# Kernel tuning notes

Hardware: AMD Instinct MI355X
Metric: run time of the kernel (lower is better)

Reference implementation:

```python
import jax, jax.numpy as jnp
import numpy as np

N_NODES = 100000
N_EDGES = 600000
D = 128


def gcn_conv(x, W, b, src, dst, n_nodes):
    """PyG-style GCNConv: add self-loops, symmetric deg^{-1/2} normalization."""
    xw = x @ W  # [N, out]
    # degree of destination nodes, counting the added self-loop
    deg = jnp.zeros((n_nodes,), xw.dtype).at[dst].add(1.0) + 1.0
    dinv = jax.lax.rsqrt(deg)
    coef = dinv[src] * dinv[dst]  # [E]
    agg = jnp.zeros_like(xw).at[dst].add(xw[src] * coef[:, None])
    agg = agg + xw * (dinv * dinv)[:, None]  # self-loop term
    return agg + b


def setup_inputs() -> dict:
    key = jax.random.key(0)
    k = jax.random.split(key, 9)
    s = 1.0 / np.sqrt(D)
    return {
        "x": jax.random.normal(k[0], (N_NODES, D), jnp.float32),
        "edge_index_pos": jax.random.randint(k[1], (2, N_EDGES), 0, N_NODES, jnp.int64),
        "edge_index_neg": jax.random.randint(k[2], (2, N_EDGES), 0, N_NODES, jnp.int64),
        "W1": jax.random.uniform(k[3], (D, D), jnp.float32, -s, s),
        "b1": jnp.zeros((D,), jnp.float32),
        "W2": jax.random.uniform(k[4], (D, D), jnp.float32, -s, s),
        "b2": jnp.zeros((D,), jnp.float32),
        "weight": jax.random.uniform(k[5], (2 * D, D), jnp.float32, -s, s),
        "bias": jnp.zeros((D,), jnp.float32),
    }


def reference(x, edge_index_pos, edge_index_neg, W1, b1, W2, b2, weight, bias):
    n = x.shape[0]
    h1 = gcn_conv(x, W1, b1, edge_index_pos[0], edge_index_pos[1], n)  # [N, D]
    h2 = gcn_conv(x, W2, b2, edge_index_neg[0], edge_index_neg[1], n)  # [N, D]
    h = jnp.concatenate([h1, h2], axis=-1)  # [N, 2D]
    return h @ weight + bias  # [N, D]
```

## Files before the change

kernel.cpp:

```cpp
#include <hip/hip_runtime.h>

#define N_NODES 100000
#define NT (2 * N_NODES)
#define D 128
#define N_EDGES 600000
#define ET (2 * N_EDGES)
#define SCAN_B 256
#define NBLK2 ((NT + SCAN_B - 1) / SCAN_B)
#define FROWS 256
#define FBLK ((N_NODES + FROWS - 1) / FROWS)
#define XBLK 12500
#define EGRID ((ET + 255) / 256)

typedef __attribute__((ext_vector_type(8))) short bf16x8;
typedef __attribute__((ext_vector_type(4))) float f32x4;

__device__ __forceinline__ unsigned short f2bf(float f) {
    union { float f; unsigned u; } v; v.f = f;
    unsigned r = (v.u + 0x7fff + ((v.u >> 16) & 1)) >> 16;
    return (unsigned short)r;
}
__device__ __forceinline__ float bf2f(unsigned short h) {
    union { unsigned u; float f; } v; v.u = ((unsigned)h) << 16;
    return v.f;
}

__device__ __forceinline__ long long load_idx(const void* e, long long i, int is32) {
    if (is32) return (long long)((const int*)e)[i];
    return ((const long long*)e)[i];
}

__device__ __forceinline__ int self_detect(const unsigned long long* __restrict__ e) {
    unsigned long long v = e[threadIdx.x & 63];
    unsigned long long m = __ballot(v > 0xFFFFFFFFull);
    return (m != 0ull) ? 1 : 0;
}

__global__ void prep_x2bf_degree(const float* __restrict__ W1, const float* __restrict__ W2,
                                 const float* __restrict__ weight,
                                 const float* __restrict__ b1, const float* __restrict__ b2,
                                 const float* __restrict__ bias,
                                 const float* __restrict__ x, unsigned short* __restrict__ xb,
                                 const void* __restrict__ ep, const void* __restrict__ en,
                                 unsigned short* __restrict__ Mt, float* __restrict__ bt,
                                 int* __restrict__ degi) {
    const int b = blockIdx.x;
    if (b < 128) {
        int idx = b * 256 + threadIdx.x;
        int j = idx >> 8, k = idx & 255;
        float a = 0.f;
        if (k < D) {
            for (int d = 0; d < D; ++d) a += W1[k * D + d] * weight[d * D + j];
        } else {
            for (int d = 0; d < D; ++d) a += W2[(k - D) * D + d] * weight[(D + d) * D + j];
        }
        Mt[j * 256 + k] = f2bf(a);
    } else if (b == 128) {
        int t = threadIdx.x;
        if (t < D) {
            float a = bias[t];
            for (int k = 0; k < D; ++k)
                a += b1[k] * weight[k * D + t] + b2[k] * weight[(D + k) * D + t];
            bt[t] = a;
        }
    } else if (b < 129 + XBLK) {
        long long t = (long long)(b - 129) * 256 + threadIdx.x;
        float4 a = ((const float4*)x)[t];
        ((ushort4*)xb)[t] = make_ushort4(f2bf(a.x), f2bf(a.y), f2bf(a.z), f2bf(a.w));
    } else {
        int is32 = self_detect((const unsigned long long*)ep);
        int i = (b - 129 - XBLK) * 256 + threadIdx.x;
        if (i >= ET) return;
        int conv = (i >= N_EDGES);
        const void* e = conv ? en : ep;
        int j = conv ? i - N_EDGES : i;
        long long d = load_idx(e, (long long)N_EDGES + j, is32);
        atomicAdd(&degi[conv * N_NODES + (int)d], 1);
    }
}

__global__ void scan_pass1(const int* __restrict__ degi, int* __restrict__ bsum,
                           float* __restrict__ dinv, unsigned char* __restrict__ degb) {
    __shared__ int sm[SCAN_B];
    int i = blockIdx.x * SCAN_B + threadIdx.x;
    int v = (i < NT) ? degi[i] : 0;
    if (i < NT) {
        dinv[i] = rsqrtf((float)v + 1.0f);
        degb[i] = (unsigned char)(v > 255 ? 255 : v);
    }
    sm[threadIdx.x] = v;
    __syncthreads();
    for (int s = SCAN_B / 2; s > 0; s >>= 1) {
        if (threadIdx.x < s) sm[threadIdx.x] += sm[threadIdx.x + s];
        __syncthreads();
    }
    if (threadIdx.x == 0) bsum[blockIdx.x] = sm[0];
}

__global__ void scan_pass3(const int* __restrict__ degi, const int* __restrict__ bsum,
                           int* __restrict__ off) {
    __shared__ int red[SCAN_B];
    __shared__ int sm[SCAN_B];
    int partial = 0;
    for (int i = threadIdx.x; i < blockIdx.x; i += SCAN_B) partial += bsum[i];
    red[threadIdx.x] = partial;
    __syncthreads();
    for (int s = SCAN_B / 2; s > 0; s >>= 1) {
        if (threadIdx.x < s) red[threadIdx.x] += red[threadIdx.x + s];
        __syncthreads();
    }
    int base = red[0];
    int i = blockIdx.x * SCAN_B + threadIdx.x;
    int v = (i < NT) ? degi[i] : 0;
    sm[threadIdx.x] = v;
    __syncthreads();
    for (int ofs = 1; ofs < SCAN_B; ofs <<= 1) {
        int add = (threadIdx.x >= ofs) ? sm[threadIdx.x - ofs] : 0;
        __syncthreads();
        sm[threadIdx.x] += add;
        __syncthreads();
    }
    int excl = sm[threadIdx.x] - v + base;
    if (i < NT) off[i] = excl;
    if (i == NT - 1) off[NT] = excl + v;
}

__global__ void csr_fill_both(const void* __restrict__ ep, const void* __restrict__ en,
                              const int* __restrict__ off,
                              int* __restrict__ degi, const unsigned char* __restrict__ degb,
                              unsigned* __restrict__ csr) {
    int is32 = self_detect((const unsigned long long*)ep);
    int i = blockIdx.x * blockDim.x + threadIdx.x;
    if (i >= ET) return;
    int conv = (i >= N_EDGES);
    const void* e = conv ? en : ep;
    int j = conv ? i - N_EDGES : i;
    int si = (int)load_idx(e, j, is32);
    int di = (int)load_idx(e, (long long)N_EDGES + j, is32);
    int g = conv * N_NODES;
    int node = g + di;
    int pos = off[node] + atomicSub(&degi[node], 1) - 1;
    unsigned degS = degb[g + si];
    csr[pos] = (unsigned)si | (degS << 20);
}

__global__ __launch_bounds__(1024) void fused_gather_gemm(
    const int* __restrict__ off, const unsigned* __restrict__ csr,
    const unsigned short* __restrict__ xb, const float* __restrict__ dinv,
    const unsigned short* __restrict__ Mt, const float* __restrict__ bt,
    float* __restrict__ out) {
    __shared__ unsigned short mlds[128][264];
    int t = threadIdx.x;
    for (int c = t; c < 4096; c += 1024) {
        int row = c >> 5;
        int kc = (c & 31) * 8;
        *(ulonglong2*)&mlds[row][kc] = *(const ulonglong2*)&Mt[row * 256 + kc];
    }
    __syncthreads();

    int wave = t >> 6, lane = t & 63;
    int rl = lane & 15, q = lane >> 4;
    int gr = blockIdx.x * FROWS + wave * 16 + rl;
    const bool valid = gr < N_NODES;

    bf16x8 af[8];
    #pragma unroll
    for (int conv = 0; conv < 2; ++conv) {
        float acc[4][8];
        if (valid) {
            int n = conv * N_NODES + gr;
            float dn = dinv[n];
            float f = dn * dn;
            const unsigned short* xr = xb + (size_t)gr * D + q * 8;
            #pragma unroll
            for (int m = 0; m < 4; ++m) {
                bf16x8 v = *(const bf16x8*)(xr + m * 32);
                #pragma unroll
                for (int j = 0; j < 8; ++j) acc[m][j] = bf2f((unsigned short)v[j]) * f;
            }
            int e0 = off[n], e1 = off[n + 1];
            int e = e0;
            for (; e + 1 < e1; e += 2) {
                unsigned c0 = csr[e], c1 = csr[e + 1];
                const unsigned short* p0 = xb + (size_t)(c0 & 0xFFFFF) * D + q * 8;
                const unsigned short* p1 = xb + (size_t)(c1 & 0xFFFFF) * D + q * 8;
                bf16x8 a0 = *(const bf16x8*)(p0);
                bf16x8 a1 = *(const bf16x8*)(p0 + 32);
                bf16x8 a2 = *(const bf16x8*)(p0 + 64);
                bf16x8 a3 = *(const bf16x8*)(p0 + 96);
                bf16x8 b0 = *(const bf16x8*)(p1);
                bf16x8 b1 = *(const bf16x8*)(p1 + 32);
                bf16x8 b2 = *(const bf16x8*)(p1 + 64);
                bf16x8 b3 = *(const bf16x8*)(p1 + 96);
                float coef0 = dn * rsqrtf((float)(c0 >> 20) + 1.0f);
                float coef1 = dn * rsqrtf((float)(c1 >> 20) + 1.0f);
                #pragma unroll
                for (int j = 0; j < 8; ++j) {
                    acc[0][j] += coef0 * bf2f((unsigned short)a0[j]);
                    acc[1][j] += coef0 * bf2f((unsigned short)a1[j]);
                    acc[2][j] += coef0 * bf2f((unsigned short)a2[j]);
                    acc[3][j] += coef0 * bf2f((unsigned short)a3[j]);
                }
                #pragma unroll
                for (int j = 0; j < 8; ++j) {
                    acc[0][j] += coef1 * bf2f((unsigned short)b0[j]);
                    acc[1][j] += coef1 * bf2f((unsigned short)b1[j]);
                    acc[2][j] += coef1 * bf2f((unsigned short)b2[j]);
                    acc[3][j] += coef1 * bf2f((unsigned short)b3[j]);
                }
            }
            if (e < e1) {
                unsigned c0 = csr[e];
                const unsigned short* p0 = xb + (size_t)(c0 & 0xFFFFF) * D + q * 8;
                bf16x8 a0 = *(const bf16x8*)(p0);
                bf16x8 a1 = *(const bf16x8*)(p0 + 32);
                bf16x8 a2 = *(const bf16x8*)(p0 + 64);
                bf16x8 a3 = *(const bf16x8*)(p0 + 96);
                float coef0 = dn * rsqrtf((float)(c0 >> 20) + 1.0f);
                #pragma unroll
                for (int j = 0; j < 8; ++j) {
                    acc[0][j] += coef0 * bf2f((unsigned short)a0[j]);
                    acc[1][j] += coef0 * bf2f((unsigned short)a1[j]);
                    acc[2][j] += coef0 * bf2f((unsigned short)a2[j]);
                    acc[3][j] += coef0 * bf2f((unsigned short)a3[j]);
                }
            }
        } else {
            #pragma unroll
            for (int m = 0; m < 4; ++m)
                #pragma unroll
                for (int j = 0; j < 8; ++j) acc[m][j] = 0.f;
        }
        #pragma unroll
        for (int m = 0; m < 4; ++m) {
            bf16x8 a;
            #pragma unroll
            for (int j = 0; j < 8; ++j) a[j] = (short)f2bf(acc[m][j]);
            af[conv * 4 + m] = a;
        }
    }

    f32x4 C[8];
    #pragma unroll
    for (int i = 0; i < 8; ++i) C[i] = (f32x4){0.f, 0.f, 0.f, 0.f};
    #pragma unroll
    for (int ks = 0; ks < 8; ++ks) {
        bf16x8 afr = af[ks];
        #pragma unroll
        for (int ct = 0; ct < 8; ++ct) {
            bf16x8 bfr = *(const bf16x8*)&mlds[ct * 16 + rl][ks * 32 + q * 8];
            C[ct] = __builtin_amdgcn_mfma_f32_16x16x32_bf16(afr, bfr, C[ct], 0, 0, 0);
        }
    }

    int orow = blockIdx.x * FROWS + wave * 16 + q * 4;
    #pragma unroll
    for (int ct = 0; ct < 8; ++ct) {
        int col = ct * 16 + rl;
        float b = bt[col];
        #pragma unroll
        for (int reg = 0; reg < 4; ++reg) {
            int row = orow + reg;
            if (row < N_NODES) out[(long long)row * D + col] = C[ct][reg] + b;
        }
    }
}

extern "C" void kernel_launch(void* const* d_in, const int* in_sizes, int n_in,
                              void* d_out, int out_size, void* d_ws, size_t ws_size,
                              hipStream_t stream) {
    const float* x      = (const float*)d_in[0];
    const void*  e_pos  = d_in[1];
    const void*  e_neg  = d_in[2];
    const float* W1     = (const float*)d_in[3];
    const float* b1     = (const float*)d_in[4];
    const float* W2     = (const float*)d_in[5];
    const float* b2     = (const float*)d_in[6];
    const float* weight = (const float*)d_in[7];
    const float* bias   = (const float*)d_in[8];
    float* out = (float*)d_out;

    unsigned short* xb = (unsigned short*)d_ws;
    unsigned short* Mt = xb + (size_t)N_NODES * D;
    float* bt   = (float*)(Mt + 128 * 256);
    float* dinv = bt + D;
    int*   degi = (int*)(dinv + NT);
    int*   off  = degi + NT;
    int*   bsum = off + NT + 4;
    unsigned char* degb = (unsigned char*)(bsum + 1024);
    unsigned* csr = (unsigned*)(degb + NT);

    hipMemsetAsync(degi, 0, NT * sizeof(int), stream);
    prep_x2bf_degree<<<129 + XBLK + EGRID, 256, 0, stream>>>(
        W1, W2, weight, b1, b2, bias, x, xb, e_pos, e_neg, Mt, bt, degi);
    scan_pass1<<<NBLK2, SCAN_B, 0, stream>>>(degi, bsum, dinv, degb);
    scan_pass3<<<NBLK2, SCAN_B, 0, stream>>>(degi, bsum, off);
    csr_fill_both<<<EGRID, 256, 0, stream>>>(e_pos, e_neg, off, degi, degb, csr);
    fused_gather_gemm<<<FBLK, 1024, 0, stream>>>(off, csr, xb, dinv, Mt, bt, out);
}
```

Measured before the change: 219.5 us.

## Prescale x by source dinv per conv and bucket CSR fill with local permutation

The source-side deg^{-1/2} factor is folded into two pre-scaled bf16 copies of x (one per conv), so the gather inner loop becomes plain adds with a single final multiply by the destination dinv. The CSR fill now uses one atomic counter per 64-node bucket, followed by an in-LDS permutation kernel that orders edges by node, which reduces atomic contention and scattered writes. In exchange it writes twice as much bf16 feature data, adds one kernel launch, and rounds x*dinv to bf16 before aggregation. The bucket permutation also caps each bucket at 1024 edges, which holds for this degree distribution but not for arbitrary graphs.

```diff
diff --git a/kernel.cpp b/kernel.cpp
--- a/kernel.cpp
+++ b/kernel.cpp
@@ -7,10 +7,11 @@
 #define ET (2 * N_EDGES)
 #define SCAN_B 256
 #define NBLK2 ((NT + SCAN_B - 1) / SCAN_B)
+#define XBLK 12500
+#define EGRID ((ET + 255) / 256)
+#define NBKT (NT / 64)
 #define FROWS 256
 #define FBLK ((N_NODES + FROWS - 1) / FROWS)
-#define XBLK 12500
-#define EGRID ((ET + 255) / 256)
 
 typedef __attribute__((ext_vector_type(8))) short bf16x8;
 typedef __attribute__((ext_vector_type(4))) float f32x4;
@@ -36,14 +37,13 @@
     return (m != 0ull) ? 1 : 0;
 }
 
-__global__ void prep_x2bf_degree(const float* __restrict__ W1, const float* __restrict__ W2,
-                                 const float* __restrict__ weight,
-                                 const float* __restrict__ b1, const float* __restrict__ b2,
-                                 const float* __restrict__ bias,
-                                 const float* __restrict__ x, unsigned short* __restrict__ xb,
-                                 const void* __restrict__ ep, const void* __restrict__ en,
-                                 unsigned short* __restrict__ Mt, float* __restrict__ bt,
-                                 int* __restrict__ degi) {
+__global__ void prep_deg(const float* __restrict__ W1, const float* __restrict__ W2,
+                         const float* __restrict__ weight,
+                         const float* __restrict__ b1, const float* __restrict__ b2,
+                         const float* __restrict__ bias,
+                         const void* __restrict__ ep, const void* __restrict__ en,
+                         unsigned short* __restrict__ Mt, float* __restrict__ bt,
+                         int* __restrict__ cnt) {
     const int b = blockIdx.x;
     if (b < 128) {
         int idx = b * 256 + threadIdx.x;
@@ -63,41 +63,47 @@
                 a += b1[k] * weight[k * D + t] + b2[k] * weight[(D + k) * D + t];
             bt[t] = a;
         }
-    } else if (b < 129 + XBLK) {
-        long long t = (long long)(b - 129) * 256 + threadIdx.x;
-        float4 a = ((const float4*)x)[t];
-        ((ushort4*)xb)[t] = make_ushort4(f2bf(a.x), f2bf(a.y), f2bf(a.z), f2bf(a.w));
     } else {
         int is32 = self_detect((const unsigned long long*)ep);
-        int i = (b - 129 - XBLK) * 256 + threadIdx.x;
+        int i = (b - 129) * 256 + threadIdx.x;
         if (i >= ET) return;
         int conv = (i >= N_EDGES);
         const void* e = conv ? en : ep;
         int j = conv ? i - N_EDGES : i;
         long long d = load_idx(e, (long long)N_EDGES + j, is32);
-        atomicAdd(&degi[conv * N_NODES + (int)d], 1);
-    }
-}
-
-__global__ void scan_pass1(const int* __restrict__ degi, int* __restrict__ bsum,
-                           float* __restrict__ dinv, unsigned char* __restrict__ degb) {
-    __shared__ int sm[SCAN_B];
-    int i = blockIdx.x * SCAN_B + threadIdx.x;
-    int v = (i < NT) ? degi[i] : 0;
-    if (i < NT) {
-        dinv[i] = rsqrtf((float)v + 1.0f);
-        degb[i] = (unsigned char)(v > 255 ? 255 : v);
-    }
-    sm[threadIdx.x] = v;
-    __syncthreads();
-    for (int s = SCAN_B / 2; s > 0; s >>= 1) {
-        if (threadIdx.x < s) sm[threadIdx.x] += sm[threadIdx.x + s];
+        atomicAdd(&cnt[conv * N_NODES + (int)d], 1);
+    }
+}
+
+__global__ void xs_scan1(const float* __restrict__ x, const int* __restrict__ cnt,
+                         unsigned short* __restrict__ xs1, unsigned short* __restrict__ xs2,
+                         int* __restrict__ bsum) {
+    if (blockIdx.x < XBLK) {
+        long long t = (long long)blockIdx.x * 256 + threadIdx.x;
+        long long row = t >> 5;
+        float d1 = rsqrtf((float)cnt[row] + 1.0f);
+        float d2 = rsqrtf((float)cnt[N_NODES + row] + 1.0f);
+        float4 a = ((const float4*)x)[t];
+        ((ushort4*)xs1)[t] = make_ushort4(f2bf(a.x * d1), f2bf(a.y * d1),
+                                          f2bf(a.z * d1), f2bf(a.w * d1));
+        ((ushort4*)xs2)[t] = make_ushort4(f2bf(a.x * d2), f2bf(a.y * d2),
+                                          f2bf(a.z * d2), f2bf(a.w * d2));
+    } else {
+        __shared__ int sm[SCAN_B];
+        int bb = blockIdx.x - XBLK;
+        int i = bb * SCAN_B + threadIdx.x;
+        int v = (i < NT) ? cnt[i] : 0;
+        sm[threadIdx.x] = v;
         __syncthreads();
-    }
-    if (threadIdx.x == 0) bsum[blockIdx.x] = sm[0];
-}
-
-__global__ void scan_pass3(const int* __restrict__ degi, const int* __restrict__ bsum,
+        for (int s = SCAN_B / 2; s > 0; s >>= 1) {
+            if (threadIdx.x < s) sm[threadIdx.x] += sm[threadIdx.x + s];
+            __syncthreads();
+        }
+        if (threadIdx.x == 0) bsum[bb] = sm[0];
+    }
+}
+
+__global__ void scan_pass3(const int* __restrict__ cnt, const int* __restrict__ bsum,
                            int* __restrict__ off) {
     __shared__ int red[SCAN_B];
     __shared__ int sm[SCAN_B];
@@ -111,7 +117,7 @@
     }
     int base = red[0];
     int i = blockIdx.x * SCAN_B + threadIdx.x;
-    int v = (i < NT) ? degi[i] : 0;
+    int v = (i < NT) ? cnt[i] : 0;
     sm[threadIdx.x] = v;
     __syncthreads();
     for (int ofs = 1; ofs < SCAN_B; ofs <<= 1) {
@@ -125,28 +131,54 @@
     if (i == NT - 1) off[NT] = excl + v;
 }
 
-__global__ void csr_fill_both(const void* __restrict__ ep, const void* __restrict__ en,
-                              const int* __restrict__ off,
-                              int* __restrict__ degi, const unsigned char* __restrict__ degb,
-                              unsigned* __restrict__ csr) {
-    int is32 = self_detect((const unsigned long long*)ep);
+__global__ void binfill(const void* __restrict__ ep_, const void* __restrict__ en_,
+                        const int* __restrict__ off, int* __restrict__ bincur,
+                        unsigned* __restrict__ csr) {
+    int is32 = self_detect((const unsigned long long*)ep_);
     int i = blockIdx.x * blockDim.x + threadIdx.x;
     if (i >= ET) return;
     int conv = (i >= N_EDGES);
-    const void* e = conv ? en : ep;
+    const void* e = conv ? en_ : ep_;
     int j = conv ? i - N_EDGES : i;
     int si = (int)load_idx(e, j, is32);
     int di = (int)load_idx(e, (long long)N_EDGES + j, is32);
-    int g = conv * N_NODES;
-    int node = g + di;
-    int pos = off[node] + atomicSub(&degi[node], 1) - 1;
-    unsigned degS = degb[g + si];
-    csr[pos] = (unsigned)si | (degS << 20);
+    int node = conv * N_NODES + di;
+    int bkt = node >> 6;
+    int base = off[node & ~63];
+    int slot = base + atomicAdd(&bincur[bkt], 1);
+    csr[slot] = (unsigned)si | ((unsigned)(node & 63) << 20);
+}
+
+__global__ void bucket_perm(const int* __restrict__ off, unsigned* __restrict__ csr) {
+    __shared__ unsigned buf[1024];
+    __shared__ int loff[64];
+    __shared__ int lcnt[64];
+    int b = blockIdx.x, t = threadIdx.x;
+    int nb = b * 64;
+    if (t < 64) {
+        int o0 = off[nb + t];
+        loff[t] = o0;
+        lcnt[t] = off[nb + t + 1] - o0;
+    }
+    __syncthreads();
+    int base = loff[0];
+    int end = loff[63] + lcnt[63];
+    int W = end - base;
+    if (W > 1024) W = 1024;
+    for (int i = t; i < W; i += 256) buf[i] = csr[base + i];
+    __syncthreads();
+    for (int i = t; i < W; i += 256) {
+        unsigned e = buf[i];
+        int d = e >> 20;
+        int sl = atomicSub(&lcnt[d], 1) - 1;
+        csr[loff[d] + sl] = e & 0xFFFFFu;
+    }
 }
 
 __global__ __launch_bounds__(1024) void fused_gather_gemm(
     const int* __restrict__ off, const unsigned* __restrict__ csr,
-    const unsigned short* __restrict__ xb, const float* __restrict__ dinv,
+    const unsigned short* __restrict__ xs1, const unsigned short* __restrict__ xs2,
+    const int* __restrict__ cnt,
     const unsigned short* __restrict__ Mt, const float* __restrict__ bt,
     float* __restrict__ out) {
     __shared__ unsigned short mlds[128][264];
@@ -166,24 +198,24 @@
     bf16x8 af[8];
     #pragma unroll
     for (int conv = 0; conv < 2; ++conv) {
+        const unsigned short* xs = conv ? xs2 : xs1;
         float acc[4][8];
         if (valid) {
             int n = conv * N_NODES + gr;
-            float dn = dinv[n];
-            float f = dn * dn;
-            const unsigned short* xr = xb + (size_t)gr * D + q * 8;
+            float dn = rsqrtf((float)cnt[n] + 1.0f);
+            const unsigned short* xr = xs + (size_t)gr * D + q * 8;
             #pragma unroll
             for (int m = 0; m < 4; ++m) {
                 bf16x8 v = *(const bf16x8*)(xr + m * 32);
                 #pragma unroll
-                for (int j = 0; j < 8; ++j) acc[m][j] = bf2f((unsigned short)v[j]) * f;
+                for (int j = 0; j < 8; ++j) acc[m][j] = bf2f((unsigned short)v[j]);
             }
             int e0 = off[n], e1 = off[n + 1];
             int e = e0;
             for (; e + 1 < e1; e += 2) {
-                unsigned c0 = csr[e], c1 = csr[e + 1];
-                const unsigned short* p0 = xb + (size_t)(c0 & 0xFFFFF) * D + q * 8;
-                const unsigned short* p1 = xb + (size_t)(c1 & 0xFFFFF) * D + q * 8;
+                unsigned s0 = csr[e], s1 = csr[e + 1];
+                const unsigned short* p0 = xs + (size_t)s0 * D + q * 8;
+                const unsigned short* p1 = xs + (size_t)s1 * D + q * 8;
                 bf16x8 a0 = *(const bf16x8*)(p0);
                 bf16x8 a1 = *(const bf16x8*)(p0 + 32);
                 bf16x8 a2 = *(const bf16x8*)(p0 + 64);
@@ -192,39 +224,40 @@
                 bf16x8 b1 = *(const bf16x8*)(p1 + 32);
                 bf16x8 b2 = *(const bf16x8*)(p1 + 64);
                 bf16x8 b3 = *(const bf16x8*)(p1 + 96);
-                float coef0 = dn * rsqrtf((float)(c0 >> 20) + 1.0f);
-                float coef1 = dn * rsqrtf((float)(c1 >> 20) + 1.0f);
                 #pragma unroll
                 for (int j = 0; j < 8; ++j) {
-                    acc[0][j] += coef0 * bf2f((unsigned short)a0[j]);
-                    acc[1][j] += coef0 * bf2f((unsigned short)a1[j]);
-                    acc[2][j] += coef0 * bf2f((unsigned short)a2[j]);
-                    acc[3][j] += coef0 * bf2f((unsigned short)a3[j]);
+                    acc[0][j] += bf2f((unsigned short)a0[j]);
+                    acc[1][j] += bf2f((unsigned short)a1[j]);
+                    acc[2][j] += bf2f((unsigned short)a2[j]);
+                    acc[3][j] += bf2f((unsigned short)a3[j]);
                 }
                 #pragma unroll
                 for (int j = 0; j < 8; ++j) {
-                    acc[0][j] += coef1 * bf2f((unsigned short)b0[j]);
-                    acc[1][j] += coef1 * bf2f((unsigned short)b1[j]);
-                    acc[2][j] += coef1 * bf2f((unsigned short)b2[j]);
-                    acc[3][j] += coef1 * bf2f((unsigned short)b3[j]);
+                    acc[0][j] += bf2f((unsigned short)b0[j]);
+                    acc[1][j] += bf2f((unsigned short)b1[j]);
+                    acc[2][j] += bf2f((unsigned short)b2[j]);
+                    acc[3][j] += bf2f((unsigned short)b3[j]);
                 }
             }
             if (e < e1) {
-                unsigned c0 = csr[e];
-                const unsigned short* p0 = xb + (size_t)(c0 & 0xFFFFF) * D + q * 8;
+                unsigned s0 = csr[e];
+                const unsigned short* p0 = xs + (size_t)s0 * D + q * 8;
                 bf16x8 a0 = *(const bf16x8*)(p0);
                 bf16x8 a1 = *(const bf16x8*)(p0 + 32);
                 bf16x8 a2 = *(const bf16x8*)(p0 + 64);
                 bf16x8 a3 = *(const bf16x8*)(p0 + 96);
-                float coef0 = dn * rsqrtf((float)(c0 >> 20) + 1.0f);
                 #pragma unroll
                 for (int j = 0; j < 8; ++j) {
-                    acc[0][j] += coef0 * bf2f((unsigned short)a0[j]);
-                    acc[1][j] += coef0 * bf2f((unsigned short)a1[j]);
-                    acc[2][j] += coef0 * bf2f((unsigned short)a2[j]);
-                    acc[3][j] += coef0 * bf2f((unsigned short)a3[j]);
+                    acc[0][j] += bf2f((unsigned short)a0[j]);
+                    acc[1][j] += bf2f((unsigned short)a1[j]);
+                    acc[2][j] += bf2f((unsigned short)a2[j]);
+                    acc[3][j] += bf2f((unsigned short)a3[j]);
                 }
             }
+            #pragma unroll
+            for (int m = 0; m < 4; ++m)
+                #pragma unroll
+                for (int j = 0; j < 8; ++j) acc[m][j] *= dn;
         } else {
             #pragma unroll
             for (int m = 0; m < 4; ++m)
@@ -280,21 +313,22 @@
     const float* bias   = (const float*)d_in[8];
     float* out = (float*)d_out;
 
-    unsigned short* xb = (unsigned short*)d_ws;
-    unsigned short* Mt = xb + (size_t)N_NODES * D;
+    unsigned short* xs1 = (unsigned short*)d_ws;
+    unsigned short* xs2 = xs1 + (size_t)N_NODES * D;
+    unsigned short* Mt  = xs2 + (size_t)N_NODES * D;
     float* bt   = (float*)(Mt + 128 * 256);
-    float* dinv = bt + D;
-    int*   degi = (int*)(dinv + NT);
-    int*   off  = degi + NT;
+    int*   cnt  = (int*)(bt + D);
+    int*   bincur = cnt + NT;
+    int*   off  = bincur + NBKT;
     int*   bsum = off + NT + 4;
-    unsigned char* degb = (unsigned char*)(bsum + 1024);
-    unsigned* csr = (unsigned*)(degb + NT);
-
-    hipMemsetAsync(degi, 0, NT * sizeof(int), stream);
-    prep_x2bf_degree<<<129 + XBLK + EGRID, 256, 0, stream>>>(
-        W1, W2, weight, b1, b2, bias, x, xb, e_pos, e_neg, Mt, bt, degi);
-    scan_pass1<<<NBLK2, SCAN_B, 0, stream>>>(degi, bsum, dinv, degb);
-    scan_pass3<<<NBLK2, SCAN_B, 0, stream>>>(degi, bsum, off);
-    csr_fill_both<<<EGRID, 256, 0, stream>>>(e_pos, e_neg, off, degi, degb, csr);
-    fused_gather_gemm<<<FBLK, 1024, 0, stream>>>(off, csr, xb, dinv, Mt, bt, out);
-}
+    unsigned* csr = (unsigned*)(bsum + 1024);
+
+    hipMemsetAsync(cnt, 0, (NT + NBKT) * sizeof(int), stream);
+    prep_deg<<<129 + EGRID, 256, 0, stream>>>(W1, W2, weight, b1, b2, bias,
+                                              e_pos, e_neg, Mt, bt, cnt);
+    xs_scan1<<<XBLK + NBLK2, 256, 0, stream>>>(x, cnt, xs1, xs2, bsum);
+    scan_pass3<<<NBLK2, SCAN_B, 0, stream>>>(cnt, bsum, off);
+    binfill<<<EGRID, 256, 0, stream>>>(e_pos, e_neg, off, bincur, csr);
+    bucket_perm<<<NBKT, 256, 0, stream>>>(off, csr);
+    fused_gather_gemm<<<FBLK, 1024, 0, stream>>>(off, csr, xs1, xs2, cnt, Mt, bt, out);
+}
```

Measured after the change: 334.4 us. +52.3%, slower.

## Partition CSR fill by destination range per XCD and unroll gather by four

Applied to the files above, without the earlier changes.

The CSR fill kernel now runs NPART*CBLK blocks, where block index mod 8 selects a destination-node range. Each block scans all edges and only handles those whose destination falls in its range. The intent is that the atomics and scattered CSR writes for a range stay within one XCD's L2, since blocks are dispatched round-robin across XCDs. The cost is that every partition reads the destination index array, so edge index traffic grows about eightfold. The gather loop also adds a 4-edge unrolled path to get more loads in flight per iteration, at the cost of extra register pressure in a 1024-thread kernel.

```diff
diff --git a/kernel.cpp b/kernel.cpp
--- a/kernel.cpp
+++ b/kernel.cpp
@@ -11,6 +11,9 @@
 #define FBLK ((N_NODES + FROWS - 1) / FROWS)
 #define XBLK 12500
 #define EGRID ((ET + 255) / 256)
+#define NPART 8
+#define PRNG (NT / NPART)
+#define CBLK 512
 
 typedef __attribute__((ext_vector_type(8))) short bf16x8;
 typedef __attribute__((ext_vector_type(4))) float f32x4;
@@ -125,23 +128,26 @@
     if (i == NT - 1) off[NT] = excl + v;
 }
 
-__global__ void csr_fill_both(const void* __restrict__ ep, const void* __restrict__ en,
-                              const int* __restrict__ off,
-                              int* __restrict__ degi, const unsigned char* __restrict__ degb,
-                              unsigned* __restrict__ csr) {
-    int is32 = self_detect((const unsigned long long*)ep);
-    int i = blockIdx.x * blockDim.x + threadIdx.x;
-    if (i >= ET) return;
-    int conv = (i >= N_EDGES);
-    const void* e = conv ? en : ep;
-    int j = conv ? i - N_EDGES : i;
-    int si = (int)load_idx(e, j, is32);
-    int di = (int)load_idx(e, (long long)N_EDGES + j, is32);
-    int g = conv * N_NODES;
-    int node = g + di;
-    int pos = off[node] + atomicSub(&degi[node], 1) - 1;
-    unsigned degS = degb[g + si];
-    csr[pos] = (unsigned)si | (degS << 20);
+__global__ void csr_fill_xcd(const void* __restrict__ ep_, const void* __restrict__ en_,
+                             const int* __restrict__ off, int* __restrict__ degi,
+                             const unsigned char* __restrict__ degb,
+                             unsigned* __restrict__ csr) {
+    int is32 = self_detect((const unsigned long long*)ep_);
+    int P = blockIdx.x & (NPART - 1);
+    int bi = blockIdx.x >> 3;
+    int lo = P * PRNG, hi = lo + PRNG;
+    for (int i = bi * 256 + threadIdx.x; i < ET; i += CBLK * 256) {
+        int conv = (i >= N_EDGES);
+        const void* e = conv ? en_ : ep_;
+        int j = conv ? i - N_EDGES : i;
+        int di = (int)load_idx(e, (long long)N_EDGES + j, is32);
+        int node = conv * N_NODES + di;
+        if (node < lo || node >= hi) continue;
+        int si = (int)load_idx(e, j, is32);
+        int pos = off[node] + atomicSub(&degi[node], 1) - 1;
+        unsigned degS = degb[conv * N_NODES + si];
+        csr[pos] = (unsigned)si | (degS << 20);
+    }
 }
 
 __global__ __launch_bounds__(1024) void fused_gather_gemm(
@@ -180,6 +186,61 @@
             }
             int e0 = off[n], e1 = off[n + 1];
             int e = e0;
+            for (; e + 3 < e1; e += 4) {
+                unsigned c0 = csr[e], c1 = csr[e + 1], c2 = csr[e + 2], c3 = csr[e + 3];
+                const unsigned short* p0 = xb + (size_t)(c0 & 0xFFFFF) * D + q * 8;
+                const unsigned short* p1 = xb + (size_t)(c1 & 0xFFFFF) * D + q * 8;
+                const unsigned short* p2 = xb + (size_t)(c2 & 0xFFFFF) * D + q * 8;
+                const unsigned short* p3 = xb + (size_t)(c3 & 0xFFFFF) * D + q * 8;
+                bf16x8 v00 = *(const bf16x8*)(p0);
+                bf16x8 v01 = *(const bf16x8*)(p0 + 32);
+                bf16x8 v02 = *(const bf16x8*)(p0 + 64);
+                bf16x8 v03 = *(const bf16x8*)(p0 + 96);
+                bf16x8 v10 = *(const bf16x8*)(p1);
+                bf16x8 v11 = *(const bf16x8*)(p1 + 32);
+                bf16x8 v12 = *(const bf16x8*)(p1 + 64);
+                bf16x8 v13 = *(const bf16x8*)(p1 + 96);
+                bf16x8 v20 = *(const bf16x8*)(p2);
+                bf16x8 v21 = *(const bf16x8*)(p2 + 32);
+                bf16x8 v22 = *(const bf16x8*)(p2 + 64);
+                bf16x8 v23 = *(const bf16x8*)(p2 + 96);
+                bf16x8 v30 = *(const bf16x8*)(p3);
+                bf16x8 v31 = *(const bf16x8*)(p3 + 32);
+                bf16x8 v32 = *(const bf16x8*)(p3 + 64);
+                bf16x8 v33 = *(const bf16x8*)(p3 + 96);
+                float f0 = dn * rsqrtf((float)(c0 >> 20) + 1.0f);
+                float f1 = dn * rsqrtf((float)(c1 >> 20) + 1.0f);
+                float f2 = dn * rsqrtf((float)(c2 >> 20) + 1.0f);
+                float f3 = dn * rsqrtf((float)(c3 >> 20) + 1.0f);
+                #pragma unroll
+                for (int j = 0; j < 8; ++j) {
+                    acc[0][j] += f0 * bf2f((unsigned short)v00[j]);
+                    acc[1][j] += f0 * bf2f((unsigned short)v01[j]);
+                    acc[2][j] += f0 * bf2f((unsigned short)v02[j]);
+                    acc[3][j] += f0 * bf2f((unsigned short)v03[j]);
+                }
+                #pragma unroll
+                for (int j = 0; j < 8; ++j) {
+                    acc[0][j] += f1 * bf2f((unsigned short)v10[j]);
+                    acc[1][j] += f1 * bf2f((unsigned short)v11[j]);
+                    acc[2][j] += f1 * bf2f((unsigned short)v12[j]);
+                    acc[3][j] += f1 * bf2f((unsigned short)v13[j]);
+                }
+                #pragma unroll
+                for (int j = 0; j < 8; ++j) {
+                    acc[0][j] += f2 * bf2f((unsigned short)v20[j]);
+                    acc[1][j] += f2 * bf2f((unsigned short)v21[j]);
+                    acc[2][j] += f2 * bf2f((unsigned short)v22[j]);
+                    acc[3][j] += f2 * bf2f((unsigned short)v23[j]);
+                }
+                #pragma unroll
+                for (int j = 0; j < 8; ++j) {
+                    acc[0][j] += f3 * bf2f((unsigned short)v30[j]);
+                    acc[1][j] += f3 * bf2f((unsigned short)v31[j]);
+                    acc[2][j] += f3 * bf2f((unsigned short)v32[j]);
+                    acc[3][j] += f3 * bf2f((unsigned short)v33[j]);
+                }
+            }
             for (; e + 1 < e1; e += 2) {
                 unsigned c0 = csr[e], c1 = csr[e + 1];
                 const unsigned short* p0 = xb + (size_t)(c0 & 0xFFFFF) * D + q * 8;
@@ -192,21 +253,21 @@
                 bf16x8 b1 = *(const bf16x8*)(p1 + 32);
                 bf16x8 b2 = *(const bf16x8*)(p1 + 64);
                 bf16x8 b3 = *(const bf16x8*)(p1 + 96);
-                float coef0 = dn * rsqrtf((float)(c0 >> 20) + 1.0f);
-                float coef1 = dn * rsqrtf((float)(c1 >> 20) + 1.0f);
-                #pragma unroll
-                for (int j = 0; j < 8; ++j) {
-                    acc[0][j] += coef0 * bf2f((unsigned short)a0[j]);
-                    acc[1][j] += coef0 * bf2f((unsigned short)a1[j]);
-                    acc[2][j] += coef0 * bf2f((unsigned short)a2[j]);
-                    acc[3][j] += coef0 * bf2f((unsigned short)a3[j]);
-                }
-                #pragma unroll
-                for (int j = 0; j < 8; ++j) {
-                    acc[0][j] += coef1 * bf2f((unsigned short)b0[j]);
-                    acc[1][j] += coef1 * bf2f((unsigned short)b1[j]);
-                    acc[2][j] += coef1 * bf2f((unsigned short)b2[j]);
-                    acc[3][j] += coef1 * bf2f((unsigned short)b3[j]);
+                float f0 = dn * rsqrtf((float)(c0 >> 20) + 1.0f);
+                float f1 = dn * rsqrtf((float)(c1 >> 20) + 1.0f);
+                #pragma unroll
+                for (int j = 0; j < 8; ++j) {
+                    acc[0][j] += f0 * bf2f((unsigned short)a0[j]);
+                    acc[1][j] += f0 * bf2f((unsigned short)a1[j]);
+                    acc[2][j] += f0 * bf2f((unsigned short)a2[j]);
+                    acc[3][j] += f0 * bf2f((unsigned short)a3[j]);
+                }
+                #pragma unroll
+                for (int j = 0; j < 8; ++j) {
+                    acc[0][j] += f1 * bf2f((unsigned short)b0[j]);
+                    acc[1][j] += f1 * bf2f((unsigned short)b1[j]);
+                    acc[2][j] += f1 * bf2f((unsigned short)b2[j]);
+                    acc[3][j] += f1 * bf2f((unsigned short)b3[j]);
                 }
             }
             if (e < e1) {
@@ -216,13 +277,13 @@
                 bf16x8 a1 = *(const bf16x8*)(p0 + 32);
                 bf16x8 a2 = *(const bf16x8*)(p0 + 64);
                 bf16x8 a3 = *(const bf16x8*)(p0 + 96);
-                float coef0 = dn * rsqrtf((float)(c0 >> 20) + 1.0f);
-                #pragma unroll
-                for (int j = 0; j < 8; ++j) {
-                    acc[0][j] += coef0 * bf2f((unsigned short)a0[j]);
-                    acc[1][j] += coef0 * bf2f((unsigned short)a1[j]);
-                    acc[2][j] += coef0 * bf2f((unsigned short)a2[j]);
-                    acc[3][j] += coef0 * bf2f((unsigned short)a3[j]);
+                float f0 = dn * rsqrtf((float)(c0 >> 20) + 1.0f);
+                #pragma unroll
+                for (int j = 0; j < 8; ++j) {
+                    acc[0][j] += f0 * bf2f((unsigned short)a0[j]);
+                    acc[1][j] += f0 * bf2f((unsigned short)a1[j]);
+                    acc[2][j] += f0 * bf2f((unsigned short)a2[j]);
+                    acc[3][j] += f0 * bf2f((unsigned short)a3[j]);
                 }
             }
         } else {
@@ -295,6 +356,6 @@
         W1, W2, weight, b1, b2, bias, x, xb, e_pos, e_neg, Mt, bt, degi);
     scan_pass1<<<NBLK2, SCAN_B, 0, stream>>>(degi, bsum, dinv, degb);
     scan_pass3<<<NBLK2, SCAN_B, 0, stream>>>(degi, bsum, off);
-    csr_fill_both<<<EGRID, 256, 0, stream>>>(e_pos, e_neg, off, degi, degb, csr);
+    csr_fill_xcd<<<NPART * CBLK, 256, 0, stream>>>(e_pos, e_neg, off, degi, degb, csr);
     fused_gather_gemm<<<FBLK, 1024, 0, stream>>>(off, csr, xb, dinv, Mt, bt, out);
 }
```

After: 237.2 us. 1.08x slower.
